# Kernel tuning notes

Hardware: AMD Instinct MI355X
Metric: run time of the kernel (lower is better)

## Reference

```python
import jax, jax.numpy as jnp
import numpy as np

N_NODES = 50000
N_EDGES = 800000
F_IN = 128          # num_features
F_HID = 128 * 3     # conv1 out
F_OUT = 256         # num_relations = num_criteria**2
N_CRIT = 16         # num_criteria


def setup_inputs() -> dict:
    key = jax.random.key(0)
    k_feat, k_edge, k_w1, k_w2 = jax.random.split(key, 4)
    features = jax.random.normal(k_feat, (N_NODES, F_IN), dtype=jnp.float32)
    edge_index = jax.random.randint(k_edge, (2, N_EDGES), 0, N_NODES, dtype=jnp.int32)
    # Glorot-ish init like dglnn.GraphConv
    W1 = jax.random.normal(k_w1, (F_IN, F_HID), dtype=jnp.float32) * (1.0 / np.sqrt(F_IN))
    b1 = jnp.zeros((F_HID,), dtype=jnp.float32)
    W2 = jax.random.normal(k_w2, (F_HID, F_OUT), dtype=jnp.float32) * (1.0 / np.sqrt(F_HID))
    b2 = jnp.zeros((F_OUT,), dtype=jnp.float32)
    return {"features": features, "W1": W1, "b1": b1, "W2": W2, "b2": b2,
            "edge_index": edge_index}


def reference(features, W1, b1, W2, b2, edge_index):
    src, dst = edge_index[0], edge_index[1]
    ones = jnp.ones((edge_index.shape[1],), dtype=features.dtype)
    # symmetric GCN norm with degrees clamped to min 1 (DGL norm='both')
    deg_out = jax.ops.segment_sum(ones, src, num_segments=N_NODES)
    deg_in = jax.ops.segment_sum(ones, dst, num_segments=N_NODES)
    out_norm = jnp.clip(deg_out, 1.0, None) ** -0.5   # [N]
    in_norm = jnp.clip(deg_in, 1.0, None) ** -0.5     # [N]

    def aggregate(h):
        # h: [N, d] -> D_in^{-1/2} A D_out^{-1/2} h  via edge gather + segment_sum
        msg = (h * out_norm[:, None])[src]                              # [E, d]
        return jax.ops.segment_sum(msg, dst, num_segments=N_NODES) * in_norm[:, None]

    # conv1: in(128) < out(384) -> aggregate first, then dense transform
    x = jax.nn.relu(aggregate(features) @ W1 + b1)      # [N, 384]
    # conv2: in(384) > out(256) -> dense transform first, then aggregate
    x = aggregate(x @ W2) + b2                          # [N, 256]
    return x.reshape(-1, N_CRIT, N_CRIT)                # [N, 16, 16]
```

## Files before the change

kernel.cpp:

```cpp
#include <hip/hip_runtime.h>
#include <hip/hip_bf16.h>

typedef float f32x4 __attribute__((ext_vector_type(4)));
typedef __bf16 bf16x8 __attribute__((ext_vector_type(8)));

#define NNODES 50000
#define NEDGES 800000
#define FIN 128
#define FHID 384
#define FOUT 256

#define SCAN_NB ((NNODES + 1023) / 1024)

#define HB 64
#define EPB (NEDGES / HB)
#define HW (NNODES / 2)

__device__ __forceinline__ float bf_lo(unsigned u) { return __uint_as_float(u << 16); }
__device__ __forceinline__ float bf_hi(unsigned u) { return __uint_as_float(u & 0xffff0000u); }
__device__ __forceinline__ unsigned short f2bf(float f) {
  unsigned u = __float_as_uint(f);
  u += 0x7fffu + ((u >> 16) & 1u);
  return (unsigned short)(u >> 16);
}

__global__ void cvt_feat_kernel(const float* __restrict__ f,
                                const float* __restrict__ onorm,
                                unsigned short* __restrict__ o, int n4) {
  int i = blockIdx.x * blockDim.x + threadIdx.x;
  if (i >= n4) return;
  float4 v = *(const float4*)(f + (size_t)i * 4);
  float w = onorm[(i * 4) >> 7];
  ushort4 r;
  r.x = f2bf(v.x * w); r.y = f2bf(v.y * w);
  r.z = f2bf(v.z * w); r.w = f2bf(v.w * w);
  *(ushort4*)(o + (size_t)i * 4) = r;
}

__global__ void wt_kernel(const float* __restrict__ W, __bf16* __restrict__ Wt, int K, int Nw) {
  int i = blockIdx.x * blockDim.x + threadIdx.x;
  if (i >= K * Nw) return;
  int k = i / Nw, n = i % Nw;
  unsigned short b = f2bf(W[i]);
  Wt[(size_t)n * K + k] = *(__bf16*)&b;
}

__global__ __launch_bounds__(256) void hist_kernel(
    const int* __restrict__ ei, unsigned* __restrict__ psrc,
    unsigned* __restrict__ pdst, unsigned short* __restrict__ rank) {
  __shared__ unsigned hist[HW];
  int b = blockIdx.x, pass = blockIdx.y, t = threadIdx.x;
  for (int i = t; i < HW; i += 256) hist[i] = 0;
  __syncthreads();
  const int* idx = ei + (pass ? NEDGES : 0) + b * EPB;
  if (pass == 0) {
    for (int i = t; i < EPB; i += 256) {
      int n = idx[i];
      atomicAdd(&hist[n >> 1], 1u << ((n & 1) << 4));
    }
  } else {
    for (int i = t; i < EPB; i += 256) {
      int n = idx[i];
      unsigned sh = (n & 1) << 4;
      unsigned old = atomicAdd(&hist[n >> 1], 1u << sh);
      rank[b * EPB + i] = (unsigned short)((old >> sh) & 0xFFFFu);
    }
  }
  __syncthreads();
  unsigned* dst = (pass ? pdst : psrc) + (size_t)b * HW;
  for (int i = t; i < HW; i += 256) dst[i] = hist[i];
}

__global__ __launch_bounds__(256) void reduce_hist(
    const unsigned* __restrict__ psrc, unsigned* __restrict__ pdst,
    int* __restrict__ din, float* __restrict__ onorm, float* __restrict__ inorm) {
  int w = blockIdx.x * blockDim.x + threadIdx.x;
  if (w >= HW) return;
  unsigned sl = 0, sh = 0;
#pragma unroll 8
  for (int b = 0; b < HB; ++b) {
    unsigned v = psrc[(size_t)b * HW + w];
    sl += v & 0xFFFFu; sh += v >> 16;
  }
  unsigned rl = 0, rh = 0;
#pragma unroll 8
  for (int b = 0; b < HB; ++b) {
    size_t o = (size_t)b * HW + w;
    unsigned v = pdst[o];
    pdst[o] = rl | (rh << 16);
    rl += v & 0xFFFFu; rh += v >> 16;
  }
  int n0 = 2 * w, n1 = 2 * w + 1;
  din[n0] = (int)rl; din[n1] = (int)rh;
  onorm[n0] = rsqrtf((float)(sl ? sl : 1u));
  onorm[n1] = rsqrtf((float)(sh ? sh : 1u));
  inorm[n0] = rsqrtf((float)(rl ? rl : 1u));
  inorm[n1] = rsqrtf((float)(rh ? rh : 1u));
}

__global__ __launch_bounds__(256) void scan_part1(const int* __restrict__ deg,
                                                  int* __restrict__ blocksums) {
  int b = blockIdx.x, t = threadIdx.x;
  int base = b * 1024 + t * 4;
  int s = 0;
  if (base + 4 <= NNODES) {
    int4 v = *(const int4*)(deg + base);
    s = v.x + v.y + v.z + v.w;
  } else {
    for (int j = 0; j < 4; ++j)
      if (base + j < NNODES) s += deg[base + j];
  }
  for (int d = 32; d >= 1; d >>= 1) s += __shfl_down(s, d, 64);
  __shared__ int ws[4];
  int lane = t & 63, w = t >> 6;
  if (lane == 0) ws[w] = s;
  __syncthreads();
  if (t == 0) blocksums[b] = ws[0] + ws[1] + ws[2] + ws[3];
}

__global__ void scan_mid(const int* __restrict__ bs, int* __restrict__ boff) {
  int t = threadIdx.x;
  int v = (t < SCAN_NB) ? bs[t] : 0;
  int x = v;
  for (int d = 1; d < 64; d <<= 1) {
    int y = __shfl_up(x, d, 64);
    if (t >= d) x += y;
  }
  if (t < SCAN_NB) boff[t] = x - v;
}

__global__ __launch_bounds__(256) void scan_part2(const int* __restrict__ deg,
                                                  const int* __restrict__ boff,
                                                  int* __restrict__ row_ptr) {
  int b = blockIdx.x, t = threadIdx.x;
  int base = b * 1024 + t * 4;
  int v0 = 0, v1 = 0, v2 = 0, v3 = 0;
  if (base + 4 <= NNODES) {
    int4 v = *(const int4*)(deg + base);
    v0 = v.x; v1 = v.y; v2 = v.z; v3 = v.w;
  } else {
    if (base + 0 < NNODES) v0 = deg[base + 0];
    if (base + 1 < NNODES) v1 = deg[base + 1];
    if (base + 2 < NNODES) v2 = deg[base + 2];
    if (base + 3 < NNODES) v3 = deg[base + 3];
  }
  int s = v0 + v1 + v2 + v3;
  int x = s;
  int lane = t & 63, w = t >> 6;
  for (int d = 1; d < 64; d <<= 1) {
    int y = __shfl_up(x, d, 64);
    if (lane >= d) x += y;
  }
  __shared__ int ws[4];
  if (lane == 63) ws[w] = x;
  __syncthreads();
  int woff = 0;
  for (int i = 0; i < w; ++i) woff += ws[i];
  int off = boff[b] + woff + (x - s);
  if (base + 0 < NNODES) { row_ptr[base + 0] = off; off += v0; }
  if (base + 1 < NNODES) { row_ptr[base + 1] = off; off += v1; }
  if (base + 2 < NNODES) { row_ptr[base + 2] = off; off += v2; }
  if (base + 3 < NNODES) { row_ptr[base + 3] = off; off += v3; }
  if (base < NNODES && base + 4 >= NNODES) row_ptr[NNODES] = off;
}

__global__ void fill_kernel(const int* __restrict__ ei,
                            const unsigned short* __restrict__ rank,
                            const unsigned* __restrict__ pdst,
                            const int* __restrict__ row_ptr,
                            int* __restrict__ csr) {
  int e = blockIdx.x * blockDim.x + threadIdx.x;
  if (e >= NEDGES) return;
  int n = ei[NEDGES + e];
  int b = e / EPB;
  unsigned base = (pdst[(size_t)b * HW + (n >> 1)] >> ((n & 1) << 4)) & 0xFFFFu;
  csr[row_ptr[n] + (int)base + (int)rank[e]] = ei[e];
}

__global__ __launch_bounds__(256) void agg1_kernel(
    const int* __restrict__ row_ptr, const int* __restrict__ csr,
    const float* __restrict__ inorm, const unsigned short* __restrict__ featb,
    unsigned short* __restrict__ aggF) {
  int node = (blockIdx.x << 2) + (threadIdx.x >> 6);
  if (node >= NNODES) return;
  int lane = threadIdx.x & 63;
  int quarter = lane >> 4;
  int fl8 = (lane & 15) << 3;
  const unsigned short* tab = featb + fl8;
  int beg = row_ptr[node], end = row_ptr[node + 1];
  float a0 = 0.f, a1 = 0.f, a2 = 0.f, a3 = 0.f, a4 = 0.f, a5 = 0.f, a6 = 0.f, a7 = 0.f;
  int e = beg;
  for (; e + 8 <= end; e += 8) {
    int s0 = csr[e + quarter];
    int s1 = csr[e + 4 + quarter];
    uint4 v0 = *(const uint4*)(tab + (size_t)s0 * FIN);
    uint4 v1 = *(const uint4*)(tab + (size_t)s1 * FIN);
    a0 += bf_lo(v0.x); a1 += bf_hi(v0.x); a2 += bf_lo(v0.y); a3 += bf_hi(v0.y);
    a4 += bf_lo(v0.z); a5 += bf_hi(v0.z); a6 += bf_lo(v0.w); a7 += bf_hi(v0.w);
    a0 += bf_lo(v1.x); a1 += bf_hi(v1.x); a2 += bf_lo(v1.y); a3 += bf_hi(v1.y);
    a4 += bf_lo(v1.z); a5 += bf_hi(v1.z); a6 += bf_lo(v1.w); a7 += bf_hi(v1.w);
  }
  for (int t = e + quarter; t < end; t += 4) {
    int s0 = csr[t];
    uint4 v0 = *(const uint4*)(tab + (size_t)s0 * FIN);
    a0 += bf_lo(v0.x); a1 += bf_hi(v0.x); a2 += bf_lo(v0.y); a3 += bf_hi(v0.y);
    a4 += bf_lo(v0.z); a5 += bf_hi(v0.z); a6 += bf_lo(v0.w); a7 += bf_hi(v0.w);
  }
  a0 += __shfl_xor(a0, 16, 64); a1 += __shfl_xor(a1, 16, 64);
  a2 += __shfl_xor(a2, 16, 64); a3 += __shfl_xor(a3, 16, 64);
  a4 += __shfl_xor(a4, 16, 64); a5 += __shfl_xor(a5, 16, 64);
  a6 += __shfl_xor(a6, 16, 64); a7 += __shfl_xor(a7, 16, 64);
  a0 += __shfl_xor(a0, 32, 64); a1 += __shfl_xor(a1, 32, 64);
  a2 += __shfl_xor(a2, 32, 64); a3 += __shfl_xor(a3, 32, 64);
  a4 += __shfl_xor(a4, 32, 64); a5 += __shfl_xor(a5, 32, 64);
  a6 += __shfl_xor(a6, 32, 64); a7 += __shfl_xor(a7, 32, 64);
  float p0 = (quarter == 0) ? a0 : (quarter == 1) ? a2 : (quarter == 2) ? a4 : a6;
  float p1 = (quarter == 0) ? a1 : (quarter == 1) ? a3 : (quarter == 2) ? a5 : a7;
  float inn = inorm[node];
  unsigned pk = (unsigned)f2bf(p0 * inn) | ((unsigned)f2bf(p1 * inn) << 16);
  *(unsigned*)(aggF + (size_t)node * FIN + fl8 + (quarter << 1)) = pk;
}

__global__ __launch_bounds__(256) void agg2_kernel(
    const int* __restrict__ row_ptr, const int* __restrict__ csr,
    const float* __restrict__ inorm, const unsigned short* __restrict__ h2s,
    const float* __restrict__ b2, float* __restrict__ out) {
  int node = (blockIdx.x << 2) + (threadIdx.x >> 6);
  if (node >= NNODES) return;
  int lane = threadIdx.x & 63;
  int half = lane >> 5;
  int fl8 = (lane & 31) << 3;
  const unsigned short* tab = h2s + fl8;
  int beg = row_ptr[node], end = row_ptr[node + 1];
  float a0 = 0.f, a1 = 0.f, a2 = 0.f, a3 = 0.f, a4 = 0.f, a5 = 0.f, a6 = 0.f, a7 = 0.f;
  int e = beg;
  for (; e + 4 <= end; e += 4) {
    int s0 = csr[e + half];
    int s1 = csr[e + 2 + half];
    uint4 v0 = *(const uint4*)(tab + (size_t)s0 * FOUT);
    uint4 v1 = *(const uint4*)(tab + (size_t)s1 * FOUT);
    a0 += bf_lo(v0.x); a1 += bf_hi(v0.x); a2 += bf_lo(v0.y); a3 += bf_hi(v0.y);
    a4 += bf_lo(v0.z); a5 += bf_hi(v0.z); a6 += bf_lo(v0.w); a7 += bf_hi(v0.w);
    a0 += bf_lo(v1.x); a1 += bf_hi(v1.x); a2 += bf_lo(v1.y); a3 += bf_hi(v1.y);
    a4 += bf_lo(v1.z); a5 += bf_hi(v1.z); a6 += bf_lo(v1.w); a7 += bf_hi(v1.w);
  }
  for (int t = e + half; t < end; t += 2) {
    int s0 = csr[t];
    uint4 v0 = *(const uint4*)(tab + (size_t)s0 * FOUT);
    a0 += bf_lo(v0.x); a1 += bf_hi(v0.x); a2 += bf_lo(v0.y); a3 += bf_hi(v0.y);
    a4 += bf_lo(v0.z); a5 += bf_hi(v0.z); a6 += bf_lo(v0.w); a7 += bf_hi(v0.w);
  }
  a0 += __shfl_xor(a0, 32, 64); a1 += __shfl_xor(a1, 32, 64);
  a2 += __shfl_xor(a2, 32, 64); a3 += __shfl_xor(a3, 32, 64);
  a4 += __shfl_xor(a4, 32, 64); a5 += __shfl_xor(a5, 32, 64);
  a6 += __shfl_xor(a6, 32, 64); a7 += __shfl_xor(a7, 32, 64);
  float q0 = half ? a4 : a0;
  float q1 = half ? a5 : a1;
  float q2 = half ? a6 : a2;
  float q3 = half ? a7 : a3;
  int f = fl8 + (half << 2);
  float inn = inorm[node];
  float4 bv = *(const float4*)(b2 + f);
  float4 r;
  r.x = fmaf(q0, inn, bv.x);
  r.y = fmaf(q1, inn, bv.y);
  r.z = fmaf(q2, inn, bv.z);
  r.w = fmaf(q3, inn, bv.w);
  *(float4*)(out + (size_t)node * FOUT + f) = r;
}

__device__ __forceinline__ f32x4 mfma16(bf16x8 a, bf16x8 b, f32x4 c) {
  return __builtin_amdgcn_mfma_f32_16x16x32_bf16(a, b, c, 0, 0, 0);
}

__global__ __launch_bounds__(256) void gemm_bf16(
    const __bf16* __restrict__ A, const __bf16* __restrict__ Bt,
    const float* __restrict__ bias, const float* __restrict__ row_scale,
    __bf16* __restrict__ C, int M, int N, int K, int relu) {
  __shared__ __attribute__((aligned(16))) __bf16 As[128 * 64];
  __shared__ __attribute__((aligned(16))) __bf16 Bs[128 * 64];
  const int tid = threadIdx.x;
  const int lane = tid & 63;
  const int wave = tid >> 6;
  const int wm = (wave >> 1) << 6;
  const int wn = (wave & 1) << 6;
  const int r16 = lane & 15;
  const int kg = lane >> 4;
  const int m0 = blockIdx.x * 128;
  const int n0 = blockIdx.y * 128;
  f32x4 acc[4][4];
#pragma unroll
  for (int m = 0; m < 4; ++m)
#pragma unroll
    for (int n = 0; n < 4; ++n) acc[m][n] = f32x4{0.f, 0.f, 0.f, 0.f};

  for (int k0 = 0; k0 < K; k0 += 64) {
    __syncthreads();
#pragma unroll
    for (int i = 0; i < 4; ++i) {
      int c = tid + (i << 8);
      int row = c >> 3;
      int col = c & 7;
      int sw = ((col ^ (row & 7)) << 3);
      int ga = m0 + row;
      uint4 av = make_uint4(0u, 0u, 0u, 0u);
      if (ga < M) av = *(const uint4*)(A + (size_t)ga * K + k0 + (col << 3));
      *(uint4*)(As + row * 64 + sw) = av;
      uint4 bv = *(const uint4*)(Bt + (size_t)(n0 + row) * K + k0 + (col << 3));
      *(uint4*)(Bs + row * 64 + sw) = bv;
    }
    __syncthreads();
#pragma unroll
    for (int kk = 0; kk < 2; ++kk) {
      int kc = (kk << 2) + kg;
      bf16x8 a[4], b[4];
#pragma unroll
      for (int m = 0; m < 4; ++m) {
        int r = wm + (m << 4) + r16;
        a[m] = *(const bf16x8*)(As + r * 64 + ((kc ^ (r & 7)) << 3));
      }
#pragma unroll
      for (int n = 0; n < 4; ++n) {
        int r = wn + (n << 4) + r16;
        b[n] = *(const bf16x8*)(Bs + r * 64 + ((kc ^ (r & 7)) << 3));
      }
#pragma unroll
      for (int m = 0; m < 4; ++m)
#pragma unroll
        for (int n = 0; n < 4; ++n)
          acc[m][n] = mfma16(a[m], b[n], acc[m][n]);
    }
  }
#pragma unroll
  for (int m = 0; m < 4; ++m) {
#pragma unroll
    for (int j = 0; j < 4; ++j) {
      int row = m0 + wm + (m << 4) + (kg << 2) + j;
      if (row < M) {
        float sc = row_scale ? row_scale[row] : 1.f;
#pragma unroll
        for (int n = 0; n < 4; ++n) {
          int col = n0 + wn + (n << 4) + r16;
          float v = acc[m][n][j] + (bias ? bias[col] : 0.f);
          if (relu) v = fmaxf(v, 0.f);
          v *= sc;
          unsigned short h = f2bf(v);
          C[(size_t)row * N + col] = *(__bf16*)&h;
        }
      }
    }
  }
}

extern "C" void kernel_launch(void* const* d_in, const int* in_sizes, int n_in,
                              void* d_out, int out_size, void* d_ws, size_t ws_size,
                              hipStream_t stream) {
  const float* features = (const float*)d_in[0];
  const float* W1 = (const float*)d_in[1];
  const float* b1 = (const float*)d_in[2];
  const float* W2 = (const float*)d_in[3];
  const float* b2 = (const float*)d_in[4];
  const int* ei = (const int*)d_in[5];
  float* out = (float*)d_out;

  char* ws = (char*)d_ws;
  size_t off = 0;
  auto alloc = [&](size_t bytes) -> void* {
    void* p = ws + off;
    off += (bytes + 255) & ~(size_t)255;
    return p;
  };
  float* onorm  = (float*)alloc((size_t)NNODES * 4);
  float* inorm  = (float*)alloc((size_t)NNODES * 4);
  int* din      = (int*)alloc((size_t)NNODES * 4);
  int* row_ptr  = (int*)alloc((size_t)(NNODES + 1) * 4);
  int* csr_src  = (int*)alloc((size_t)NEDGES * 4);
  int* blocksums = (int*)alloc((size_t)SCAN_NB * 4);
  int* blockoffs = (int*)alloc((size_t)SCAN_NB * 4);
  unsigned short* featb = (unsigned short*)alloc((size_t)NNODES * FIN * 2);
  unsigned short* aggF  = (unsigned short*)alloc((size_t)NNODES * FIN * 2);
  __bf16* h1  = (__bf16*)alloc((size_t)NNODES * FHID * 2);
  __bf16* h2s = (__bf16*)alloc((size_t)NNODES * FOUT * 2);
  __bf16* W1t = (__bf16*)alloc((size_t)FIN * FHID * 2);
  __bf16* W2t = (__bf16*)alloc((size_t)FHID * FOUT * 2);
  (void)ws_size; (void)n_in; (void)in_sizes; (void)out_size;

  unsigned* psrc = (unsigned*)h1;
  unsigned* pdst = psrc + (size_t)HB * HW;
  unsigned short* rank = (unsigned short*)(pdst + (size_t)HB * HW);

  hist_kernel<<<dim3(HB, 2), 256, 0, stream>>>(ei, psrc, pdst, rank);
  reduce_hist<<<(HW + 255) / 256, 256, 0, stream>>>(psrc, pdst, din, onorm, inorm);
  scan_part1<<<SCAN_NB, 256, 0, stream>>>(din, blocksums);
  scan_mid<<<1, 64, 0, stream>>>(blocksums, blockoffs);
  scan_part2<<<SCAN_NB, 256, 0, stream>>>(din, blockoffs, row_ptr);
  fill_kernel<<<(NEDGES + 255) / 256, 256, 0, stream>>>(ei, rank, pdst, row_ptr, csr_src);

  cvt_feat_kernel<<<(NNODES * FIN / 4 + 255) / 256, 256, 0, stream>>>(
      features, onorm, featb, NNODES * FIN / 4);
  wt_kernel<<<(FIN * FHID + 255) / 256, 256, 0, stream>>>(W1, W1t, FIN, FHID);
  wt_kernel<<<(FHID * FOUT + 255) / 256, 256, 0, stream>>>(W2, W2t, FHID, FOUT);

  agg1_kernel<<<(NNODES + 3) / 4, 256, 0, stream>>>(
      row_ptr, csr_src, inorm, featb, aggF);
  gemm_bf16<<<dim3((NNODES + 127) / 128, FHID / 128), 256, 0, stream>>>(
      (const __bf16*)aggF, W1t, b1, nullptr, h1, NNODES, FHID, FIN, 1);

  gemm_bf16<<<dim3((NNODES + 127) / 128, FOUT / 128), 256, 0, stream>>>(
      h1, W2t, nullptr, onorm, h2s, NNODES, FOUT, FHID, 0);
  agg2_kernel<<<(NNODES + 3) / 4, 256, 0, stream>>>(
      row_ptr, csr_src, inorm, (const unsigned short*)h2s, b2, out);
}
```

Measured before the change: 313.2 us.

## Split aggregation kernels into feature panels with 16 edges per wave in parallel

Both aggregation kernels now split the feature dimension into 32-column panels, one panel per workgroup, so a wave reads only 64 bytes per source row but covers 16 edges at once instead of 2 or 4. The launch grid grows 4x for agg1 and 8x for agg2. The aim is more memory requests in flight per wave and better latency hiding on the random gathers. In exchange, the CSR indices and row pointers are re-read once per panel, reductions take more shuffle steps, and only a quarter of the lanes do the final write.

New measurement: 434.4 us. 1.39x slower.

```diff
diff --git a/kernel.cpp b/kernel.cpp
--- a/kernel.cpp
+++ b/kernel.cpp
@@ -181,92 +181,81 @@
     const int* __restrict__ row_ptr, const int* __restrict__ csr,
     const float* __restrict__ inorm, const unsigned short* __restrict__ featb,
     unsigned short* __restrict__ aggF) {
-  int node = (blockIdx.x << 2) + (threadIdx.x >> 6);
+  int wgid = blockIdx.x;
+  int panel = wgid & 3;
+  int node = ((wgid >> 2) << 2) + (threadIdx.x >> 6);
   if (node >= NNODES) return;
   int lane = threadIdx.x & 63;
-  int quarter = lane >> 4;
-  int fl8 = (lane & 15) << 3;
-  const unsigned short* tab = featb + fl8;
+  int es = lane >> 2;
+  int fl = lane & 3;
+  const unsigned short* tab = featb + panel * 32 + fl * 8;
   int beg = row_ptr[node], end = row_ptr[node + 1];
   float a0 = 0.f, a1 = 0.f, a2 = 0.f, a3 = 0.f, a4 = 0.f, a5 = 0.f, a6 = 0.f, a7 = 0.f;
-  int e = beg;
-  for (; e + 8 <= end; e += 8) {
-    int s0 = csr[e + quarter];
-    int s1 = csr[e + 4 + quarter];
-    uint4 v0 = *(const uint4*)(tab + (size_t)s0 * FIN);
-    uint4 v1 = *(const uint4*)(tab + (size_t)s1 * FIN);
-    a0 += bf_lo(v0.x); a1 += bf_hi(v0.x); a2 += bf_lo(v0.y); a3 += bf_hi(v0.y);
-    a4 += bf_lo(v0.z); a5 += bf_hi(v0.z); a6 += bf_lo(v0.w); a7 += bf_hi(v0.w);
-    a0 += bf_lo(v1.x); a1 += bf_hi(v1.x); a2 += bf_lo(v1.y); a3 += bf_hi(v1.y);
-    a4 += bf_lo(v1.z); a5 += bf_hi(v1.z); a6 += bf_lo(v1.w); a7 += bf_hi(v1.w);
-  }
-  for (int t = e + quarter; t < end; t += 4) {
-    int s0 = csr[t];
-    uint4 v0 = *(const uint4*)(tab + (size_t)s0 * FIN);
-    a0 += bf_lo(v0.x); a1 += bf_hi(v0.x); a2 += bf_lo(v0.y); a3 += bf_hi(v0.y);
-    a4 += bf_lo(v0.z); a5 += bf_hi(v0.z); a6 += bf_lo(v0.w); a7 += bf_hi(v0.w);
-  }
-  a0 += __shfl_xor(a0, 16, 64); a1 += __shfl_xor(a1, 16, 64);
-  a2 += __shfl_xor(a2, 16, 64); a3 += __shfl_xor(a3, 16, 64);
-  a4 += __shfl_xor(a4, 16, 64); a5 += __shfl_xor(a5, 16, 64);
-  a6 += __shfl_xor(a6, 16, 64); a7 += __shfl_xor(a7, 16, 64);
-  a0 += __shfl_xor(a0, 32, 64); a1 += __shfl_xor(a1, 32, 64);
-  a2 += __shfl_xor(a2, 32, 64); a3 += __shfl_xor(a3, 32, 64);
-  a4 += __shfl_xor(a4, 32, 64); a5 += __shfl_xor(a5, 32, 64);
-  a6 += __shfl_xor(a6, 32, 64); a7 += __shfl_xor(a7, 32, 64);
-  float p0 = (quarter == 0) ? a0 : (quarter == 1) ? a2 : (quarter == 2) ? a4 : a6;
-  float p1 = (quarter == 0) ? a1 : (quarter == 1) ? a3 : (quarter == 2) ? a5 : a7;
-  float inn = inorm[node];
-  unsigned pk = (unsigned)f2bf(p0 * inn) | ((unsigned)f2bf(p1 * inn) << 16);
-  *(unsigned*)(aggF + (size_t)node * FIN + fl8 + (quarter << 1)) = pk;
+  for (int e = beg + es; e < end; e += 16) {
+    int s = csr[e];
+    uint4 v = *(const uint4*)(tab + (size_t)s * FIN);
+    a0 += bf_lo(v.x); a1 += bf_hi(v.x); a2 += bf_lo(v.y); a3 += bf_hi(v.y);
+    a4 += bf_lo(v.z); a5 += bf_hi(v.z); a6 += bf_lo(v.w); a7 += bf_hi(v.w);
+  }
+#pragma unroll
+  for (int d = 4; d <= 32; d <<= 1) {
+    a0 += __shfl_xor(a0, d, 64); a1 += __shfl_xor(a1, d, 64);
+    a2 += __shfl_xor(a2, d, 64); a3 += __shfl_xor(a3, d, 64);
+    a4 += __shfl_xor(a4, d, 64); a5 += __shfl_xor(a5, d, 64);
+    a6 += __shfl_xor(a6, d, 64); a7 += __shfl_xor(a7, d, 64);
+  }
+  if (es == 0) {
+    float inn = inorm[node];
+    uint4 pk;
+    pk.x = (unsigned)f2bf(a0 * inn) | ((unsigned)f2bf(a1 * inn) << 16);
+    pk.y = (unsigned)f2bf(a2 * inn) | ((unsigned)f2bf(a3 * inn) << 16);
+    pk.z = (unsigned)f2bf(a4 * inn) | ((unsigned)f2bf(a5 * inn) << 16);
+    pk.w = (unsigned)f2bf(a6 * inn) | ((unsigned)f2bf(a7 * inn) << 16);
+    *(uint4*)(aggF + (size_t)node * FIN + panel * 32 + fl * 8) = pk;
+  }
 }
 
 __global__ __launch_bounds__(256) void agg2_kernel(
     const int* __restrict__ row_ptr, const int* __restrict__ csr,
     const float* __restrict__ inorm, const unsigned short* __restrict__ h2s,
     const float* __restrict__ b2, float* __restrict__ out) {
-  int node = (blockIdx.x << 2) + (threadIdx.x >> 6);
+  int wgid = blockIdx.x;
+  int panel = wgid & 7;
+  int node = ((wgid >> 3) << 2) + (threadIdx.x >> 6);
   if (node >= NNODES) return;
   int lane = threadIdx.x & 63;
-  int half = lane >> 5;
-  int fl8 = (lane & 31) << 3;
-  const unsigned short* tab = h2s + fl8;
+  int es = lane >> 2;
+  int fl = lane & 3;
+  const unsigned short* tab = h2s + panel * 32 + fl * 8;
   int beg = row_ptr[node], end = row_ptr[node + 1];
   float a0 = 0.f, a1 = 0.f, a2 = 0.f, a3 = 0.f, a4 = 0.f, a5 = 0.f, a6 = 0.f, a7 = 0.f;
-  int e = beg;
-  for (; e + 4 <= end; e += 4) {
-    int s0 = csr[e + half];
-    int s1 = csr[e + 2 + half];
-    uint4 v0 = *(const uint4*)(tab + (size_t)s0 * FOUT);
-    uint4 v1 = *(const uint4*)(tab + (size_t)s1 * FOUT);
-    a0 += bf_lo(v0.x); a1 += bf_hi(v0.x); a2 += bf_lo(v0.y); a3 += bf_hi(v0.y);
-    a4 += bf_lo(v0.z); a5 += bf_hi(v0.z); a6 += bf_lo(v0.w); a7 += bf_hi(v0.w);
-    a0 += bf_lo(v1.x); a1 += bf_hi(v1.x); a2 += bf_lo(v1.y); a3 += bf_hi(v1.y);
-    a4 += bf_lo(v1.z); a5 += bf_hi(v1.z); a6 += bf_lo(v1.w); a7 += bf_hi(v1.w);
-  }
-  for (int t = e + half; t < end; t += 2) {
-    int s0 = csr[t];
-    uint4 v0 = *(const uint4*)(tab + (size_t)s0 * FOUT);
-    a0 += bf_lo(v0.x); a1 += bf_hi(v0.x); a2 += bf_lo(v0.y); a3 += bf_hi(v0.y);
-    a4 += bf_lo(v0.z); a5 += bf_hi(v0.z); a6 += bf_lo(v0.w); a7 += bf_hi(v0.w);
-  }
-  a0 += __shfl_xor(a0, 32, 64); a1 += __shfl_xor(a1, 32, 64);
-  a2 += __shfl_xor(a2, 32, 64); a3 += __shfl_xor(a3, 32, 64);
-  a4 += __shfl_xor(a4, 32, 64); a5 += __shfl_xor(a5, 32, 64);
-  a6 += __shfl_xor(a6, 32, 64); a7 += __shfl_xor(a7, 32, 64);
-  float q0 = half ? a4 : a0;
-  float q1 = half ? a5 : a1;
-  float q2 = half ? a6 : a2;
-  float q3 = half ? a7 : a3;
-  int f = fl8 + (half << 2);
-  float inn = inorm[node];
-  float4 bv = *(const float4*)(b2 + f);
-  float4 r;
-  r.x = fmaf(q0, inn, bv.x);
-  r.y = fmaf(q1, inn, bv.y);
-  r.z = fmaf(q2, inn, bv.z);
-  r.w = fmaf(q3, inn, bv.w);
-  *(float4*)(out + (size_t)node * FOUT + f) = r;
+  for (int e = beg + es; e < end; e += 16) {
+    int s = csr[e];
+    uint4 v = *(const uint4*)(tab + (size_t)s * FOUT);
+    a0 += bf_lo(v.x); a1 += bf_hi(v.x); a2 += bf_lo(v.y); a3 += bf_hi(v.y);
+    a4 += bf_lo(v.z); a5 += bf_hi(v.z); a6 += bf_lo(v.w); a7 += bf_hi(v.w);
+  }
+#pragma unroll
+  for (int d = 4; d <= 32; d <<= 1) {
+    a0 += __shfl_xor(a0, d, 64); a1 += __shfl_xor(a1, d, 64);
+    a2 += __shfl_xor(a2, d, 64); a3 += __shfl_xor(a3, d, 64);
+    a4 += __shfl_xor(a4, d, 64); a5 += __shfl_xor(a5, d, 64);
+    a6 += __shfl_xor(a6, d, 64); a7 += __shfl_xor(a7, d, 64);
+  }
+  if (es == 0) {
+    int f = panel * 32 + fl * 8;
+    float inn = inorm[node];
+    float4 b0 = *(const float4*)(b2 + f);
+    float4 b1 = *(const float4*)(b2 + f + 4);
+    float4 r0, r1;
+    r0.x = fmaf(a0, inn, b0.x); r0.y = fmaf(a1, inn, b0.y);
+    r0.z = fmaf(a2, inn, b0.z); r0.w = fmaf(a3, inn, b0.w);
+    r1.x = fmaf(a4, inn, b1.x); r1.y = fmaf(a5, inn, b1.y);
+    r1.z = fmaf(a6, inn, b1.z); r1.w = fmaf(a7, inn, b1.w);
+    float* op = out + (size_t)node * FOUT + f;
+    *(float4*)op = r0;
+    *(float4*)(op + 4) = r1;
+  }
 }
 
 __device__ __forceinline__ f32x4 mfma16(bf16x8 a, bf16x8 b, f32x4 c) {
@@ -401,13 +390,13 @@
   wt_kernel<<<(FIN * FHID + 255) / 256, 256, 0, stream>>>(W1, W1t, FIN, FHID);
   wt_kernel<<<(FHID * FOUT + 255) / 256, 256, 0, stream>>>(W2, W2t, FHID, FOUT);
 
-  agg1_kernel<<<(NNODES + 3) / 4, 256, 0, stream>>>(
+  agg1_kernel<<<((NNODES + 3) / 4) * 4, 256, 0, stream>>>(
       row_ptr, csr_src, inorm, featb, aggF);
   gemm_bf16<<<dim3((NNODES + 127) / 128, FHID / 128), 256, 0, stream>>>(
       (const __bf16*)aggF, W1t, b1, nullptr, h1, NNODES, FHID, FIN, 1);
 
   gemm_bf16<<<dim3((NNODES + 127) / 128, FOUT / 128), 256, 0, stream>>>(
       h1, W2t, nullptr, onorm, h2s, NNODES, FOUT, FHID, 0);
-  agg2_kernel<<<(NNODES + 3) / 4, 256, 0, stream>>>(
+  agg2_kernel<<<((NNODES + 3) / 4) * 8, 256, 0, stream>>>(
       row_ptr, csr_src, inorm, (const unsigned short*)h2s, b2, out);
 }
```
